# Kernel optimization log

Measured on AMD Instinct MI355X. Metric: run time of the kernel, lower is better.

Reference implementation:

```python
import jax, jax.numpy as jnp
import numpy as np

BLOCK_SIZE = 32
# E2M1 (FP4) representable magnitudes and rounding midpoints
FP4_GRID = jnp.array([0.0, 0.5, 1.0, 1.5, 2.0, 3.0, 4.0, 6.0], dtype=jnp.float32)
FP4_MIDS = jnp.array([0.25, 0.75, 1.25, 1.75, 2.5, 3.5, 5.0], dtype=jnp.float32)


def quantize_to_mxfp4(w, block_size=BLOCK_SIZE):
    """Quantize (K, N) weight to MXFP4: per-block-of-32 (along K) power-of-2 scale
    + E2M1 codes. Returns dequantized-code tensor q (K//bs, bs, N) and scales
    (K//bs, 1, N) so that dequant = q * scales."""
    K, N = w.shape
    wb = w.reshape(K // block_size, block_size, N)
    amax = jnp.max(jnp.abs(wb), axis=1, keepdims=True)          # (K//bs, 1, N)
    # E8M0 scale: 2^(floor(log2(amax)) - 2) so amax/scale falls in [4, 8) -> clipped to 6
    exp = jnp.floor(jnp.log2(jnp.maximum(amax, 1e-30))) - 2.0
    scales = jnp.exp2(exp)
    x = wb / scales
    idx = jnp.digitize(jnp.abs(x), FP4_MIDS)                    # round-to-nearest FP4 magnitude
    q = jnp.sign(x) * FP4_GRID[idx]
    return q, scales


def mxfp4_matmul(inputs, q, scales, block_size=BLOCK_SIZE):
    """inputs: (..., K); q: (K//bs, bs, N); scales: (K//bs, 1, N)."""
    K = inputs.shape[-1]
    N = q.shape[-1]
    w = (q * scales).reshape(K, N)   # fused dequant (reference form)
    return inputs @ w


def setup_inputs() -> dict:
    key = jax.random.key(0)
    ks = jax.random.split(key, 3)
    B, S, D, F = 4, 2048, 2048, 8192
    inputs = jax.random.normal(ks[0], (B, S, D), dtype=jnp.float32)
    up_kernel = jax.random.normal(ks[1], (D, F), dtype=jnp.float32) * (1.0 / np.sqrt(D))
    down_kernel = jax.random.normal(ks[2], (F, D), dtype=jnp.float32) * (1.0 / np.sqrt(F))
    up_bias = jnp.zeros((F,), dtype=jnp.float32)
    down_bias = jnp.zeros((D,), dtype=jnp.float32)
    return {"inputs": inputs, "up_kernel": up_kernel, "up_bias": up_bias,
            "down_kernel": down_kernel, "down_bias": down_bias}


def reference(inputs, up_kernel, up_bias, down_kernel, down_bias):
    q_up, s_up = quantize_to_mxfp4(up_kernel, BLOCK_SIZE)
    x = mxfp4_matmul(inputs, q_up, s_up, BLOCK_SIZE) + up_bias
    x = jax.nn.gelu(x)
    q_dn, s_dn = quantize_to_mxfp4(down_kernel, BLOCK_SIZE)
    x = mxfp4_matmul(x, q_dn, s_dn, BLOCK_SIZE) + down_bias
    return x
```

## Files before the change

### kernel.cpp

```cpp
#include <hip/hip_runtime.h>
#include <hip/hip_bf16.h>

typedef __bf16 bf16_t;
typedef __attribute__((ext_vector_type(8))) __bf16 bf16x8;
typedef __attribute__((ext_vector_type(4))) float f32x4;
typedef __attribute__((ext_vector_type(4))) unsigned int u32x4;

__device__ __forceinline__ void gload_lds16(const bf16_t* g, bf16_t* l) {
    __builtin_amdgcn_global_load_lds(
        (const __attribute__((address_space(1))) void*)g,
        (__attribute__((address_space(3))) void*)l,
        16, 0, 0);
}

__device__ __forceinline__ float gelu_f(float v) {
    float u = 0.7978845608028654f * (v + 0.044715f * v * v * v);
    float e = __expf(-2.f * u);
    float t = __fdividef(1.f - e, 1.f + e);
    return 0.5f * v * (1.f + t);
}

__device__ __forceinline__ void quant_one(const float* __restrict__ w,
                                          bf16_t* __restrict__ wt,
                                          int K, int N, int tix) {
    int n = tix % N;
    int b = tix / N;
    const float* src = w + (size_t)b * 32 * N + n;
    float v[32];
    float amax = 0.f;
#pragma unroll
    for (int i = 0; i < 32; ++i) {
        v[i] = __builtin_nontemporal_load(src + (size_t)i * N);
        amax = fmaxf(amax, fabsf(v[i]));
    }
    unsigned eb = (__float_as_uint(amax) >> 23) & 0xFF;
    float scale = __uint_as_float((eb - 2u) << 23);
    float inv   = __uint_as_float((256u - eb) << 23);
    if (amax == 0.f) { scale = 0.f; inv = 0.f; }
    bf16_t dq[32];
#pragma unroll
    for (int i = 0; i < 32; ++i) {
        float x  = v[i] * inv;
        float ax = fabsf(x);
        float q = ax < 0.25f ? 0.0f : ax < 0.75f ? 0.5f : ax < 1.25f ? 1.0f :
                  ax < 1.75f ? 1.5f : ax < 2.5f  ? 2.0f : ax < 3.5f  ? 3.0f :
                  ax < 5.0f  ? 4.0f : 6.0f;
        float d = copysignf(q * scale, x);
        dq[i] = (bf16_t)d;
    }
    const int r  = n & 255, rt = n >> 8, kt = b >> 1, ub = (b & 1) * 4;
    bf16_t* base = wt + (((size_t)rt * (K >> 6) + kt) << 14) + (r << 6);
#pragma unroll
    for (int j = 0; j < 4; ++j) {
        bf16x8 p;
#pragma unroll
        for (int t = 0; t < 8; ++t) p[t] = dq[j * 8 + t];
        *(bf16x8*)(base + (((ub + j) ^ (r & 7)) << 3)) = p;
    }
}

__global__ void prep_kernel(const float* __restrict__ in, bf16_t* __restrict__ out,
                            int ncvt, int cvtB, int dLog,
                            const float* __restrict__ upw, bf16_t* __restrict__ upwt,
                            int upK, int upN, int qupB,
                            const float* __restrict__ dnw, bf16_t* __restrict__ dnwt,
                            int dnK, int dnN) {
    int bid = blockIdx.x;
    if (bid < cvtB) {
        int i = (bid * blockDim.x + threadIdx.x) << 3;
        if (i >= ncvt) return;
        const f32x4* p = (const f32x4*)(in + i);
        f32x4 a = __builtin_nontemporal_load(p);
        f32x4 b = __builtin_nontemporal_load(p + 1);
        bf16x8 o;
        o[0] = (bf16_t)a[0]; o[1] = (bf16_t)a[1]; o[2] = (bf16_t)a[2]; o[3] = (bf16_t)a[3];
        o[4] = (bf16_t)b[0]; o[5] = (bf16_t)b[1]; o[6] = (bf16_t)b[2]; o[7] = (bf16_t)b[3];
        const int row = i >> dLog, d = i & ((1 << dLog) - 1);
        const int r = row & 255, mt = row >> 8, dt = d >> 6, u = (d >> 3) & 7;
        size_t off = (((size_t)mt * (1 << (dLog - 6)) + dt) << 14) + (r << 6)
                     + ((u ^ (r & 7)) << 3);
        *(bf16x8*)(out + off) = o;
    } else if (bid < cvtB + qupB) {
        int tix = (bid - cvtB) * blockDim.x + threadIdx.x;
        if (tix >= (upK >> 5) * upN) return;
        quant_one(upw, upwt, upK, upN, tix);
    } else {
        int tix = (bid - cvtB - qupB) * blockDim.x + threadIdx.x;
        if (tix >= (dnK >> 5) * dnN) return;
        quant_one(dnw, dnwt, dnK, dnN, tix);
    }
}

#define VMW4  asm volatile("s_waitcnt vmcnt(4)" ::: "memory")
#define VMW0  asm volatile("s_waitcnt vmcnt(0)" ::: "memory")
#define BARR  asm volatile("s_barrier" ::: "memory")
#define LGKM0 asm volatile("s_waitcnt lgkmcnt(0)" ::: "memory")

__global__ __launch_bounds__(512, 4)
void gemm1_kernel(const bf16_t* __restrict__ A, const bf16_t* __restrict__ Bt,
                  const float* __restrict__ bias, bf16_t* __restrict__ C,
                  int M, int N, int K) {
    __shared__ __align__(16) char smem[65536];
    bf16_t* sAp = (bf16_t*)smem;
    bf16_t* sBp = (bf16_t*)(smem + 32768);
    const int tid     = threadIdx.x;
    const int lane    = tid & 63;
    const int wv      = tid >> 6;
    const int wr      = wv >> 1;
    const int wc      = wv & 1;
    const int laneLow = lane & 15;
    const int laneHi  = lane >> 4;

    const int bid = blockIdx.x;
    const int xcd = bid & 7, l = bid >> 3, r = l >> 5, u = l & 31;
    const int bm = ((xcd & 1) << 3) + (u >> 2) + ((r & 1) << 4);
    const int bn = ((xcd >> 1) << 2) + (u & 3) + ((r >> 1) << 4);

    const int kT = K >> 6;
    const int rtB = bn >> 1;
    const size_t bHalf = (size_t)(bn & 1) << 13;

    auto stageA = [&](int kt) {
        const bf16_t* s = A + (((size_t)bm * kT + kt) << 14)
                            + ((wv * 8) << 6) + lane * 8;
#pragma unroll
        for (int h = 0; h < 2; ++h) {
            gload_lds16(s + h * 8192,        &sAp[(h * 128 + wv * 8) * 64]);
            gload_lds16(s + h * 8192 + 4096, &sAp[(h * 128 + 64 + wv * 8) * 64]);
        }
    };
    auto stageB = [&](int kt) {
        const bf16_t* s = Bt + (((size_t)rtB * kT + kt) << 14) + bHalf
                             + ((wv * 8) << 6) + lane * 8;
        gload_lds16(s,        &sBp[(wv * 8) * 64]);
        gload_lds16(s + 4096, &sBp[(64 + wv * 8) * 64]);
    };

    const int s7  = laneLow & 7;
    const int xk0 = ((laneHi) ^ s7) << 3;
    const int xk1 = ((4 + laneHi) ^ s7) << 3;
    const int aOffBase = (wr * 64 + laneLow) * 64;
    const int bOffBase = (wc * 64 + laneLow) * 64;

    f32x4 acc[4][4];
#pragma unroll
    for (int i = 0; i < 4; ++i)
#pragma unroll
        for (int j = 0; j < 4; ++j) acc[i][j] = (f32x4){0.f, 0.f, 0.f, 0.f};

#pragma unroll 1
    for (int kt = 0; kt < kT; ++kt) {
        stageA(kt); stageB(kt);
        VMW0;
        BARR;
        __builtin_amdgcn_s_setprio(1);
#pragma unroll
        for (int ks = 0; ks < 2; ++ks) {
            const int xk = ks ? xk1 : xk0;
            bf16x8 b0 = *(const bf16x8*)(&sBp[bOffBase + 0 * 1024 + xk]);
            bf16x8 b1 = *(const bf16x8*)(&sBp[bOffBase + 1 * 1024 + xk]);
            bf16x8 b2 = *(const bf16x8*)(&sBp[bOffBase + 2 * 1024 + xk]);
            bf16x8 b3 = *(const bf16x8*)(&sBp[bOffBase + 3 * 1024 + xk]);
#pragma unroll
            for (int m = 0; m < 4; ++m) {
                bf16x8 a = *(const bf16x8*)(&sAp[aOffBase + m * 1024 + xk]);
                acc[m][0] = __builtin_amdgcn_mfma_f32_16x16x32_bf16(a, b0, acc[m][0], 0, 0, 0);
                acc[m][1] = __builtin_amdgcn_mfma_f32_16x16x32_bf16(a, b1, acc[m][1], 0, 0, 0);
                acc[m][2] = __builtin_amdgcn_mfma_f32_16x16x32_bf16(a, b2, acc[m][2], 0, 0, 0);
                acc[m][3] = __builtin_amdgcn_mfma_f32_16x16x32_bf16(a, b3, acc[m][3], 0, 0, 0);
            }
        }
        __builtin_amdgcn_s_setprio(0);
        BARR;
    }

    char* sC = smem;
#pragma unroll
    for (int n = 0; n < 4; ++n) {
        const int colL = wc * 64 + n * 16 + laneLow;
        const float bv = bias[bn * 128 + colL];
        const int u6   = (colL >> 3) & 7;
#pragma unroll
        for (int m = 0; m < 4; ++m) {
#pragma unroll
            for (int j = 0; j < 4; ++j) {
                const int rowL = wr * 64 + m * 16 + (laneHi << 2) + j;
                float v = acc[m][n][j] + bv;
                int byte = ((colL >> 6) << 15) + (rowL << 7)
                         + ((u6 ^ (rowL & 7)) << 4) + ((colL & 7) << 1);
                byte ^= ((rowL >> 2) & 3) << 5;
                *(bf16_t*)(sC + byte) = (bf16_t)gelu_f(v);
            }
        }
    }
    LGKM0;
    BARR;
    char* dst = (char*)C + (((size_t)bm * (N >> 6) + bn * 2) << 15);
#pragma unroll
    for (int s = 0; s < 8; ++s) {
        int lin = s * 8192 + tid * 16;
        int row = (lin >> 7) & 255;
        int rb  = lin ^ (((row >> 2) & 3) << 5);
        u32x4 v = *(const u32x4*)(sC + rb);
        __builtin_nontemporal_store(v, (u32x4*)(dst + lin));
    }
}

#define MFMA_ROW(MI, A0, A1)                                                          \
    acc[MI][0] = __builtin_amdgcn_mfma_f32_16x16x32_bf16(A0, bf00, acc[MI][0],0,0,0); \
    acc[MI][0] = __builtin_amdgcn_mfma_f32_16x16x32_bf16(A1, bf01, acc[MI][0],0,0,0); \
    acc[MI][1] = __builtin_amdgcn_mfma_f32_16x16x32_bf16(A0, bf10, acc[MI][1],0,0,0); \
    acc[MI][1] = __builtin_amdgcn_mfma_f32_16x16x32_bf16(A1, bf11, acc[MI][1],0,0,0); \
    acc[MI][2] = __builtin_amdgcn_mfma_f32_16x16x32_bf16(A0, bf20, acc[MI][2],0,0,0); \
    acc[MI][2] = __builtin_amdgcn_mfma_f32_16x16x32_bf16(A1, bf21, acc[MI][2],0,0,0); \
    acc[MI][3] = __builtin_amdgcn_mfma_f32_16x16x32_bf16(A0, bf30, acc[MI][3],0,0,0); \
    acc[MI][3] = __builtin_amdgcn_mfma_f32_16x16x32_bf16(A1, bf31, acc[MI][3],0,0,0);

#define PHASE(BUF, P, STAGE_STMT, TAIL_STMT)                                          \
  {                                                                                   \
    af00 = lda(BUF, 2*(P),   0); af01 = lda(BUF, 2*(P),   1);                         \
    af10 = lda(BUF, 2*(P)+1, 0); af11 = lda(BUF, 2*(P)+1, 1);                         \
    if ((P) == 0) {                                                                   \
      bf00 = ldb(BUF,0,0); bf01 = ldb(BUF,0,1);                                       \
      bf10 = ldb(BUF,1,0); bf11 = ldb(BUF,1,1);                                       \
      bf20 = ldb(BUF,2,0); bf21 = ldb(BUF,2,1);                                       \
      bf30 = ldb(BUF,3,0); bf31 = ldb(BUF,3,1);                                       \
    }                                                                                 \
    STAGE_STMT;                                                                       \
    BARR;                                                                             \
    LGKM0;                                                                            \
    __builtin_amdgcn_s_setprio(1);                                                    \
    MFMA_ROW(2*(P),   af00, af01);                                                    \
    MFMA_ROW(2*(P)+1, af10, af11);                                                    \
    __builtin_amdgcn_s_setprio(0);                                                    \
    TAIL_STMT;                                                                        \
    BARR;                                                                             \
  }

__global__ __launch_bounds__(512, 2)
void gemm2_kernel(const bf16_t* __restrict__ A, const bf16_t* __restrict__ Bt,
                  const float* __restrict__ bias, float* __restrict__ Cf,
                  int M, int N, int K) {
    __shared__ __align__(16) char smem[131072];
    bf16_t* sAp = (bf16_t*)smem;
    bf16_t* sBp = (bf16_t*)(smem + 65536);
    const int tid     = threadIdx.x;
    const int lane    = tid & 63;
    const int wv      = tid >> 6;
    const int wr      = wv >> 2;
    const int wc      = wv & 3;
    const int laneLow = lane & 15;
    const int laneHi  = lane >> 4;

    const int ntn = N >> 8;
    const int nwg = gridDim.x;
    const int bid = blockIdx.x;
    int wg  = (bid & 7) * (nwg >> 3) + (bid >> 3);
    const int bm = wg / ntn, bn = wg % ntn;

    const int kT = K >> 6;

    auto stageA = [&](int b, int kt, int h) {
        const bf16_t* s = A + (((size_t)bm * kT + kt) << 14)
                            + ((h * 128 + wv * 8) << 6) + lane * 8;
        gload_lds16(s,        &sAp[b * 16384 + (h * 128 + wv * 8) * 64]);
        gload_lds16(s + 4096, &sAp[b * 16384 + (h * 128 + 64 + wv * 8) * 64]);
    };
    auto stageB = [&](int b, int kt, int h) {
        const bf16_t* s = Bt + (((size_t)bn * kT + kt) << 14)
                             + ((h * 128 + wv * 8) << 6) + lane * 8;
        gload_lds16(s,        &sBp[b * 16384 + (h * 128 + wv * 8) * 64]);
        gload_lds16(s + 4096, &sBp[b * 16384 + (h * 128 + 64 + wv * 8) * 64]);
    };

    const int s7  = laneLow & 7;
    const int xk0 = ((laneHi) ^ s7) << 3;
    const int xk1 = ((4 + laneHi) ^ s7) << 3;
    const int aOffBase = (wr * 128 + laneLow) * 64;
    const int bOffBase = (wc * 64 + laneLow) * 64;
    auto lda = [&](int b, int m, int ks) -> bf16x8 {
        return *(const bf16x8*)(&sAp[b * 16384 + aOffBase + m * 1024 + (ks ? xk1 : xk0)]);
    };
    auto ldb = [&](int b, int n2, int ks) -> bf16x8 {
        return *(const bf16x8*)(&sBp[b * 16384 + bOffBase + n2 * 1024 + (ks ? xk1 : xk0)]);
    };

    f32x4 acc[8][4];
#pragma unroll
    for (int i = 0; i < 8; ++i)
#pragma unroll
        for (int j = 0; j < 4; ++j) acc[i][j] = (f32x4){0.f, 0.f, 0.f, 0.f};

    bf16x8 af00, af01, af10, af11;
    bf16x8 bf00, bf01, bf10, bf11, bf20, bf21, bf30, bf31;

    stageA(0, 0, 0); stageA(0, 0, 1);
    stageB(0, 0, 0); stageB(0, 0, 1);
    stageB(1, 1, 0); stageB(1, 1, 1);
    VMW4;
    BARR;

    const int niter = kT >> 1;
    for (int i = 0; i < niter; ++i) {
        const bool nlast = (i + 1 < niter);
        const int kO  = 2 * i + 1;
        const int kN  = 2 * i + 2;
        const int kN1 = 2 * i + 3;
        PHASE(0, 0, stageA(1, kO, 0), ((void)0));
        PHASE(0, 1, stageA(1, kO, 1), ((void)0));
        PHASE(0, 2, if (nlast) stageB(0, kN, 0), ((void)0));
        PHASE(0, 3, if (nlast) stageB(0, kN, 1),
              if (nlast) { VMW4; } else { VMW0; });
        PHASE(1, 0, if (nlast) stageA(0, kN, 0), ((void)0));
        PHASE(1, 1, if (nlast) stageA(0, kN, 1), ((void)0));
        PHASE(1, 2, if (nlast) stageB(1, kN1, 0), ((void)0));
        PHASE(1, 3, if (nlast) stageB(1, kN1, 1),
              if (nlast) { VMW4; });
    }

    const int r0 = bm * 256 + wr * 128 + (laneHi << 2);
    const int c0 = bn * 256 + wc * 64 + laneLow;
#pragma unroll
    for (int n = 0; n < 4; ++n) {
        const int col = c0 + n * 16;
        const float bv = bias[col];
#pragma unroll
        for (int m = 0; m < 8; ++m) {
#pragma unroll
            for (int j = 0; j < 4; ++j) {
                const int row = r0 + m * 16 + j;
                __builtin_nontemporal_store(acc[m][n][j] + bv,
                                            &Cf[(size_t)row * N + col]);
            }
        }
    }
}

extern "C" void kernel_launch(void* const* d_in, const int* in_sizes, int n_in,
                              void* d_out, int out_size, void* d_ws, size_t ws_size,
                              hipStream_t stream) {
    const float* inputs = (const float*)d_in[0];
    const float* up_w   = (const float*)d_in[1];
    const float* up_b   = (const float*)d_in[2];
    const float* dn_w   = (const float*)d_in[3];
    const float* dn_b   = (const float*)d_in[4];
    float* out = (float*)d_out;

    const int D = in_sizes[4];
    const int F = in_sizes[2];
    const int M = in_sizes[0] / D;
    const int dLog = 31 - __builtin_clz((unsigned)D);

    size_t r0_bytes = (size_t)(M > F ? M : F) * D * 2;
    char* ws = (char*)d_ws;
    bf16_t* in_bf = (bf16_t*)ws;
    bf16_t* wup_t = (bf16_t*)(ws + r0_bytes);
    bf16_t* mid   = (bf16_t*)(ws + r0_bytes + (size_t)F * D * 2);
    bf16_t* wdn_t = (bf16_t*)(ws + r0_bytes + (size_t)F * D * 2 + (size_t)M * F * 2);

    int ncvt = M * D;
    int cvtB = ncvt / (8 * 256);
    int qupB = ((D / 32) * F + 255) / 256;
    int qdnB = ((F / 32) * D + 255) / 256;
    prep_kernel<<<cvtB + qupB + qdnB, 256, 0, stream>>>(
        inputs, in_bf, ncvt, cvtB, dLog,
        up_w, wup_t, D, F, qupB,
        dn_w, wdn_t, F, D);

    gemm1_kernel<<<(M / 256) * (F / 128), 512, 0, stream>>>(
        in_bf, wup_t, up_b, mid, M, F, D);

    gemm2_kernel<<<(M / 256) * (D / 256), 512, 0, stream>>>(
        mid, wdn_t, dn_b, out, M, D, F);
    (void)ws_size; (void)n_in; (void)out_size;
}
```

Measured before the change: 531.6 us.

## Load A fragments directly into registers and double-buffer B in gemm1

The prep kernel now writes the bf16 activations in a per-lane fragment layout, so each wave can load its A operands straight from global memory into registers instead of staging them through LDS. B tiles are double-buffered in LDS and the next tile's A and B loads are issued while the current tile's MFMAs run, with partial vmcnt waits. This aims to remove the full load-wait-compute serialization and the LDS traffic for A. The cost is more VGPR pressure, duplicated A global reads across the two column waves, and more complex wait-count bookkeeping.

```diff
diff --git a/kernel.cpp b/kernel.cpp
--- a/kernel.cpp
+++ b/kernel.cpp
@@ -5,6 +5,7 @@
 typedef __attribute__((ext_vector_type(8))) __bf16 bf16x8;
 typedef __attribute__((ext_vector_type(4))) float f32x4;
 typedef __attribute__((ext_vector_type(4))) unsigned int u32x4;
+typedef const __attribute__((address_space(1))) u32x4* gbl_u32x4p;
 
 __device__ __forceinline__ void gload_lds16(const bf16_t* g, bf16_t* l) {
     __builtin_amdgcn_global_load_lds(
@@ -76,9 +77,11 @@
         o[0] = (bf16_t)a[0]; o[1] = (bf16_t)a[1]; o[2] = (bf16_t)a[2]; o[3] = (bf16_t)a[3];
         o[4] = (bf16_t)b[0]; o[5] = (bf16_t)b[1]; o[6] = (bf16_t)b[2]; o[7] = (bf16_t)b[3];
         const int row = i >> dLog, d = i & ((1 << dLog) - 1);
-        const int r = row & 255, mt = row >> 8, dt = d >> 6, u = (d >> 3) & 7;
-        size_t off = (((size_t)mt * (1 << (dLog - 6)) + dt) << 14) + (r << 6)
-                     + ((u ^ (r & 7)) << 3);
+        const int mt = row >> 8, rl = row & 255;
+        const int wr = rl >> 6, m = (rl >> 4) & 3, lL = rl & 15;
+        const int kt = d >> 6, ks = (d >> 5) & 1, lH = (d >> 3) & 3;
+        size_t off = (((size_t)mt * (1 << (dLog - 6)) + kt) << 14)
+                   + (((((wr << 2) + m) << 1) + ks) << 9) + (((lH << 4) + lL) << 3);
         *(bf16x8*)(out + off) = o;
     } else if (bid < cvtB + qupB) {
         int tix = (bid - cvtB) * blockDim.x + threadIdx.x;
@@ -91,18 +94,20 @@
     }
 }
 
+#define VMW8  asm volatile("s_waitcnt vmcnt(8)" ::: "memory")
+#define VMW6  asm volatile("s_waitcnt vmcnt(6)" ::: "memory")
 #define VMW4  asm volatile("s_waitcnt vmcnt(4)" ::: "memory")
 #define VMW0  asm volatile("s_waitcnt vmcnt(0)" ::: "memory")
 #define BARR  asm volatile("s_barrier" ::: "memory")
 #define LGKM0 asm volatile("s_waitcnt lgkmcnt(0)" ::: "memory")
+#define SB0   __builtin_amdgcn_sched_barrier(0)
 
 __global__ __launch_bounds__(512, 4)
-void gemm1_kernel(const bf16_t* __restrict__ A, const bf16_t* __restrict__ Bt,
+void gemm1_kernel(const bf16_t* __restrict__ Areg, const bf16_t* __restrict__ Bt,
                   const float* __restrict__ bias, bf16_t* __restrict__ C,
                   int M, int N, int K) {
     __shared__ __align__(16) char smem[65536];
-    bf16_t* sAp = (bf16_t*)smem;
-    bf16_t* sBp = (bf16_t*)(smem + 32768);
+    bf16_t* sBp = (bf16_t*)smem;
     const int tid     = threadIdx.x;
     const int lane    = tid & 63;
     const int wv      = tid >> 6;
@@ -120,26 +125,22 @@
     const int rtB = bn >> 1;
     const size_t bHalf = (size_t)(bn & 1) << 13;
 
-    auto stageA = [&](int kt) {
-        const bf16_t* s = A + (((size_t)bm * kT + kt) << 14)
-                            + ((wv * 8) << 6) + lane * 8;
-#pragma unroll
-        for (int h = 0; h < 2; ++h) {
-            gload_lds16(s + h * 8192,        &sAp[(h * 128 + wv * 8) * 64]);
-            gload_lds16(s + h * 8192 + 4096, &sAp[(h * 128 + 64 + wv * 8) * 64]);
-        }
-    };
-    auto stageB = [&](int kt) {
+    auto aSrc = [&](int kt, int m, int ks) -> gbl_u32x4p {
+        return (gbl_u32x4p)(const void*)(
+            Areg + (((size_t)bm * kT + kt) << 14)
+                 + (((((wr << 2) + m) << 1) + ks) << 9));
+    };
+    auto stageB = [&](int buf, int kt) {
         const bf16_t* s = Bt + (((size_t)rtB * kT + kt) << 14) + bHalf
                              + ((wv * 8) << 6) + lane * 8;
-        gload_lds16(s,        &sBp[(wv * 8) * 64]);
-        gload_lds16(s + 4096, &sBp[(64 + wv * 8) * 64]);
+        bf16_t* d = sBp + buf * 8192;
+        gload_lds16(s,        d + (wv * 8) * 64);
+        gload_lds16(s + 4096, d + (64 + wv * 8) * 64);
     };
 
     const int s7  = laneLow & 7;
     const int xk0 = ((laneHi) ^ s7) << 3;
     const int xk1 = ((4 + laneHi) ^ s7) << 3;
-    const int aOffBase = (wr * 64 + laneLow) * 64;
     const int bOffBase = (wc * 64 + laneLow) * 64;
 
     f32x4 acc[4][4];
@@ -147,32 +148,68 @@
     for (int i = 0; i < 4; ++i)
 #pragma unroll
         for (int j = 0; j < 4; ++j) acc[i][j] = (f32x4){0.f, 0.f, 0.f, 0.f};
+
+    u32x4 a0, a1, a2, a3, a4, a5, a6, a7;
+
+#define G1_HALF(XK, A0_, A1_, A2_, A3_)                                           \
+    {                                                                             \
+        const bf16_t* sBc = sBp + cur * 8192;                                     \
+        bf16x8 b0 = *(const bf16x8*)(&sBc[bOffBase + 0 * 1024 + (XK)]);           \
+        bf16x8 b1 = *(const bf16x8*)(&sBc[bOffBase + 1 * 1024 + (XK)]);           \
+        bf16x8 b2 = *(const bf16x8*)(&sBc[bOffBase + 2 * 1024 + (XK)]);           \
+        bf16x8 b3 = *(const bf16x8*)(&sBc[bOffBase + 3 * 1024 + (XK)]);           \
+        bf16x8 f0 = __builtin_bit_cast(bf16x8, A0_);                              \
+        bf16x8 f1 = __builtin_bit_cast(bf16x8, A1_);                              \
+        bf16x8 f2 = __builtin_bit_cast(bf16x8, A2_);                              \
+        bf16x8 f3 = __builtin_bit_cast(bf16x8, A3_);                              \
+        acc[0][0] = __builtin_amdgcn_mfma_f32_16x16x32_bf16(f0, b0, acc[0][0], 0, 0, 0); \
+        acc[0][1] = __builtin_amdgcn_mfma_f32_16x16x32_bf16(f0, b1, acc[0][1], 0, 0, 0); \
+        acc[0][2] = __builtin_amdgcn_mfma_f32_16x16x32_bf16(f0, b2, acc[0][2], 0, 0, 0); \
+        acc[0][3] = __builtin_amdgcn_mfma_f32_16x16x32_bf16(f0, b3, acc[0][3], 0, 0, 0); \
+        acc[1][0] = __builtin_amdgcn_mfma_f32_16x16x32_bf16(f1, b0, acc[1][0], 0, 0, 0); \
+        acc[1][1] = __builtin_amdgcn_mfma_f32_16x16x32_bf16(f1, b1, acc[1][1], 0, 0, 0); \
+        acc[1][2] = __builtin_amdgcn_mfma_f32_16x16x32_bf16(f1, b2, acc[1][2], 0, 0, 0); \
+        acc[1][3] = __builtin_amdgcn_mfma_f32_16x16x32_bf16(f1, b3, acc[1][3], 0, 0, 0); \
+        acc[2][0] = __builtin_amdgcn_mfma_f32_16x16x32_bf16(f2, b0, acc[2][0], 0, 0, 0); \
+        acc[2][1] = __builtin_amdgcn_mfma_f32_16x16x32_bf16(f2, b1, acc[2][1], 0, 0, 0); \
+        acc[2][2] = __builtin_amdgcn_mfma_f32_16x16x32_bf16(f2, b2, acc[2][2], 0, 0, 0); \
+        acc[2][3] = __builtin_amdgcn_mfma_f32_16x16x32_bf16(f2, b3, acc[2][3], 0, 0, 0); \
+        acc[3][0] = __builtin_amdgcn_mfma_f32_16x16x32_bf16(f3, b0, acc[3][0], 0, 0, 0); \
+        acc[3][1] = __builtin_amdgcn_mfma_f32_16x16x32_bf16(f3, b1, acc[3][1], 0, 0, 0); \
+        acc[3][2] = __builtin_amdgcn_mfma_f32_16x16x32_bf16(f3, b2, acc[3][2], 0, 0, 0); \
+        acc[3][3] = __builtin_amdgcn_mfma_f32_16x16x32_bf16(f3, b3, acc[3][3], 0, 0, 0); \
+    }
+
+    stageB(0, 0);
+    a0 = aSrc(0, 0, 0)[lane]; a1 = aSrc(0, 1, 0)[lane];
+    a2 = aSrc(0, 2, 0)[lane]; a3 = aSrc(0, 3, 0)[lane];
+    a4 = aSrc(0, 0, 1)[lane]; a5 = aSrc(0, 1, 1)[lane];
+    a6 = aSrc(0, 2, 1)[lane]; a7 = aSrc(0, 3, 1)[lane];
+    VMW8;
+    BARR;
+    int cur = 0;
 
 #pragma unroll 1
     for (int kt = 0; kt < kT; ++kt) {
-        stageA(kt); stageB(kt);
-        VMW0;
+        const int nx = (kt + 1 < kT) ? kt + 1 : kt;
+        stageB(cur ^ 1, nx);
+        VMW6; SB0;
+        __builtin_amdgcn_s_setprio(1);
+        G1_HALF(xk0, a0, a1, a2, a3);
+        __builtin_amdgcn_s_setprio(0);
+        a0 = aSrc(nx, 0, 0)[lane]; a1 = aSrc(nx, 1, 0)[lane];
+        a2 = aSrc(nx, 2, 0)[lane]; a3 = aSrc(nx, 3, 0)[lane];
+        VMW6; SB0;
+        __builtin_amdgcn_s_setprio(1);
+        G1_HALF(xk1, a4, a5, a6, a7);
+        __builtin_amdgcn_s_setprio(0);
+        a4 = aSrc(nx, 0, 1)[lane]; a5 = aSrc(nx, 1, 1)[lane];
+        a6 = aSrc(nx, 2, 1)[lane]; a7 = aSrc(nx, 3, 1)[lane];
+        VMW8;
         BARR;
-        __builtin_amdgcn_s_setprio(1);
-#pragma unroll
-        for (int ks = 0; ks < 2; ++ks) {
-            const int xk = ks ? xk1 : xk0;
-            bf16x8 b0 = *(const bf16x8*)(&sBp[bOffBase + 0 * 1024 + xk]);
-            bf16x8 b1 = *(const bf16x8*)(&sBp[bOffBase + 1 * 1024 + xk]);
-            bf16x8 b2 = *(const bf16x8*)(&sBp[bOffBase + 2 * 1024 + xk]);
-            bf16x8 b3 = *(const bf16x8*)(&sBp[bOffBase + 3 * 1024 + xk]);
-#pragma unroll
-            for (int m = 0; m < 4; ++m) {
-                bf16x8 a = *(const bf16x8*)(&sAp[aOffBase + m * 1024 + xk]);
-                acc[m][0] = __builtin_amdgcn_mfma_f32_16x16x32_bf16(a, b0, acc[m][0], 0, 0, 0);
-                acc[m][1] = __builtin_amdgcn_mfma_f32_16x16x32_bf16(a, b1, acc[m][1], 0, 0, 0);
-                acc[m][2] = __builtin_amdgcn_mfma_f32_16x16x32_bf16(a, b2, acc[m][2], 0, 0, 0);
-                acc[m][3] = __builtin_amdgcn_mfma_f32_16x16x32_bf16(a, b3, acc[m][3], 0, 0, 0);
-            }
-        }
-        __builtin_amdgcn_s_setprio(0);
-        BARR;
-    }
+        cur ^= 1;
+    }
+#undef G1_HALF
 
     char* sC = smem;
 #pragma unroll
```

New measurement: 667.1 us. 25.5% more time.
